# Kernel tuning notes

Measured on AMD Instinct MI355X. Metric: run time of the kernel, lower is better.

The kernel has to match this reference:

```python
import jax, jax.numpy as jnp
import numpy as np

BN_EPS = 1e-5
K = 3  # kernel size


def conv2d(x, w, b, pad):
    y = jax.lax.conv_general_dilated(
        x, w, window_strides=(1, 1), padding=[(pad, pad), (pad, pad)],
        dimension_numbers=('NCHW', 'OIHW', 'NCHW'))
    return y + b[None, :, None, None]


def setup_inputs() -> dict:
    key = jax.random.key(0)
    ks = jax.random.split(key, 4)
    B, C, H, W, O = 8, 256, 64, 64, 256
    x = jax.random.normal(ks[0], (B, C, H, W), dtype=jnp.float32)
    # offset/mask conv: 3*dg*k*k = 27 out channels; small init -> small offsets
    w_off = jax.random.normal(ks[1], (27, C, K, K), dtype=jnp.float32) * 0.01
    b_off = jnp.zeros((27,), dtype=jnp.float32)
    # main deformable conv weight/bias
    w = jax.random.normal(ks[2], (O, C, K, K), dtype=jnp.float32) * 0.05
    b = jnp.zeros((O,), dtype=jnp.float32)
    # BatchNorm (inference) params / running stats
    gamma = jnp.ones((O,), dtype=jnp.float32)
    beta = jnp.zeros((O,), dtype=jnp.float32)
    run_mean = jnp.zeros((O,), dtype=jnp.float32)
    run_var = jnp.ones((O,), dtype=jnp.float32)
    return {"x": x, "w_off": w_off, "b_off": b_off, "w": w, "b": b,
            "gamma": gamma, "beta": beta, "run_mean": run_mean, "run_var": run_var}


def _dcn_bn_relu(x, w_off, b_off, w, b, gamma, beta, run_mean, run_var):
    B, C, H, W = x.shape
    KK = K * K
    # offset + modulation mask (DCNv2): channels [0:9]=dy, [9:18]=dx, [18:27]=mask
    om = conv2d(x, w_off, b_off, pad=1)            # [B, 27, H, W]
    dy, dx = om[:, :KK], om[:, KK:2 * KK]          # [B, 9, H, W]
    mod = jax.nn.sigmoid(om[:, 2 * KK:])           # [B, 9, H, W]

    ky, kx = jnp.meshgrid(jnp.arange(K), jnp.arange(K), indexing='ij')
    # base sampling grid: out pixel + dilation*(k - center), padding=1
    base_y = jnp.arange(H, dtype=jnp.float32)[None, :, None] - 1.0 + ky.reshape(KK, 1, 1)
    base_x = jnp.arange(W, dtype=jnp.float32)[None, None, :] - 1.0 + kx.reshape(KK, 1, 1)
    py = base_y[None] + dy                          # [B, 9, H, W]
    px = base_x[None] + dx

    y0 = jnp.floor(py); x0 = jnp.floor(px)
    fy = py - y0; fx = px - x0
    y0 = y0.astype(jnp.int32); x0 = x0.astype(jnp.int32)

    x_flat = x.reshape(B, C, H * W)
    gather = jax.vmap(lambda xf, idx: xf[:, idx])   # ([C,HW],[9,H,W]) -> [C,9,H,W]

    def corner(yi, xi, wgt):
        valid = (yi >= 0) & (yi < H) & (xi >= 0) & (xi < W)
        idx = jnp.clip(yi, 0, H - 1) * W + jnp.clip(xi, 0, W - 1)
        val = gather(x_flat, idx)                   # [B, C, 9, H, W]
        return val * (wgt * valid.astype(wgt.dtype))[:, None]

    sampled = (corner(y0,     x0,     (1 - fy) * (1 - fx))
               + corner(y0,     x0 + 1, (1 - fy) * fx)
               + corner(y0 + 1, x0,     fy * (1 - fx))
               + corner(y0 + 1, x0 + 1, fy * fx))    # [B, C, 9, H, W]
    sampled = sampled * mod[:, None]                 # modulation

    O = w.shape[0]
    out = jnp.einsum('bckhw,ock->bohw', sampled, w.reshape(O, C, KK))
    out = out + b[None, :, None, None]

    # BatchNorm2d (inference) + ReLU
    inv = gamma / jnp.sqrt(run_var + BN_EPS)
    out = out * inv[None, :, None, None] + (beta - run_mean * inv)[None, :, None, None]
    return jax.nn.relu(out)


def reference(x, w_off, b_off, w, b, gamma, beta, run_mean, run_var):
    return _dcn_bn_relu(x, w_off, b_off, w, b, gamma, beta, run_mean, run_var)
```

## Files before the change

kernel.cpp:

```cpp
#include <hip/hip_runtime.h>
#include <math.h>

#define B_   8
#define C_   256
#define H_   64
#define W_   64
#define O_   256
#define KK_  9
#define CK_  2304
#define HW_  4096
#define BN_EPS 1e-5f

typedef __bf16 bf16x8 __attribute__((ext_vector_type(8)));
typedef float  f32x4  __attribute__((ext_vector_type(4)));

static __device__ __forceinline__ unsigned short f2bf(float f) {
    unsigned int u = __float_as_uint(f);
    unsigned int r = (u + 0x7fffu + ((u >> 16) & 1u)) >> 16;
    return (unsigned short)r;
}
static __device__ __forceinline__ float bflo(unsigned int u) {
    return __uint_as_float(u << 16);
}
static __device__ __forceinline__ float bfhi(unsigned int u) {
    return __uint_as_float(u & 0xffff0000u);
}
static __device__ __forceinline__ unsigned int pack2bf(float a, float b) {
    return (unsigned int)f2bf(a) | ((unsigned int)f2bf(b) << 16);
}

__global__ __launch_bounds__(256) void prep_kernel(
    const float* __restrict__ x, const float* __restrict__ w,
    const float* __restrict__ w_off,
    unsigned short* __restrict__ xT, unsigned short* __restrict__ wKf,
    unsigned short* __restrict__ wof)
{
    int blk = blockIdx.x;
    if (blk < 2048) {
        __shared__ float tile[64][65];
        const int b   = blk & 7;
        const int ct  = (blk >> 3) & 3;
        const int hwt = blk >> 5;
        const int c0  = ct * 64, hw0 = hwt * 64;
        const int tl  = threadIdx.x & 63, tg = threadIdx.x >> 6;
#pragma unroll
        for (int r = 0; r < 16; ++r) {
            int c_l = tg + r * 4;
            tile[c_l][tl] = x[((size_t)(b * C_ + c0 + c_l)) * HW_ + hw0 + tl];
        }
        __syncthreads();
#pragma unroll
        for (int r = 0; r < 16; ++r) {
            int hw_l = tg + r * 4;
            xT[((size_t)(b * HW_ + hw0 + hw_l)) * C_ + c0 + tl] = f2bf(tile[tl][hw_l]);
        }
    } else if (blk < 2048 + 2304) {
        int idx = (blk - 2048) * 256 + threadIdx.x;
        int o   = idx / CK_;
        int rem = idx - o * CK_;
        int c   = rem / 9;
        int tap = rem - c * 9;
        int NT  = o >> 4, n16 = o & 15;
        int kap = tap * 256 + c;
        int KC  = kap >> 5, kr = kap & 31;
        int lane = ((kr >> 3) << 4) | n16, e = kr & 7;
        wKf[((size_t)(NT * 72 + KC) * 64 + lane) * 8 + e] = f2bf(w[idx]);
    } else {
        int idx = (blk - 4352) * 256 + threadIdx.x;
        int NT  = idx / 36864;
        int r   = idx - NT * 36864;
        int KC  = r >> 9;
        int r2  = r & 511;
        int lane = r2 >> 3, e = r2 & 7;
        int n16 = lane & 15, q = lane >> 4;
        int o   = NT * 16 + n16;
        int kap = KC * 32 + q * 8 + e;
        int tap = kap >> 8, c = kap & 255;
        wof[idx] = (o < 27) ? f2bf(w_off[(o * C_ + c) * KK_ + tap])
                            : (unsigned short)0;
    }
}

__global__ __launch_bounds__(512) void offset_mfma_kernel(
    const unsigned short* __restrict__ xT, const unsigned short* __restrict__ wof,
    const float* __restrict__ b_off, float* __restrict__ om)
{
    __shared__ unsigned short rowbuf[66 * 264];

    const int blk = blockIdx.x;
    const int b = blk & 7, h = blk >> 3;
    const int tid = threadIdx.x, lane = tid & 63, wv = tid >> 6;
    const int mi = wv & 3, nj = wv >> 2;
    const int m16 = lane & 15, q = lane >> 4;

    f32x4 acc = {0.f, 0.f, 0.f, 0.f};
    const uint4* wof4 = (const uint4*)wof;

    for (int r = 0; r < 3; ++r) {
        const int hh = h - 1 + r;
        const bool vr = (hh >= 0) && (hh < H_);
        __syncthreads();
        if (vr) {
            const uint4* src = (const uint4*)&xT[((size_t)(b * HW_ + hh * W_)) * C_];
#pragma unroll
            for (int i = 0; i < 8; ++i) {
                int idx8 = i * 512 + tid;
                int px = idx8 >> 5, c8 = (idx8 & 31) * 8;
                *(uint4*)&rowbuf[(px + 1) * 264 + c8] = src[idx8];
            }
        }
        if (tid < 33) {
            *(uint4*)&rowbuf[tid * 8] = make_uint4(0u, 0u, 0u, 0u);
        } else if (tid >= 256 && tid < 289) {
            *(uint4*)&rowbuf[65 * 264 + (tid - 256) * 8] = make_uint4(0u, 0u, 0u, 0u);
        }
        __syncthreads();
        if (vr) {
            for (int s = 0; s < 3; ++s) {
                const unsigned short* arow = &rowbuf[(mi * 16 + m16 + s) * 264 + q * 8];
#pragma unroll
                for (int cc = 0; cc < 8; ++cc) {
                    bf16x8 a = *(const bf16x8*)&arow[cc * 32];
                    const int KC = (r * 3 + s) * 8 + cc;
                    uint4 braw = wof4[(size_t)(nj * 72 + KC) * 64 + lane];
                    acc = __builtin_amdgcn_mfma_f32_16x16x32_bf16(
                        a, __builtin_bit_cast(bf16x8, braw), acc, 0, 0, 0);
                }
            }
        }
    }

    const int t = nj * 16 + m16;
    if (t < 27) {
        const float bo = b_off[t];
        float s0 = acc[0] + bo, s1 = acc[1] + bo, s2 = acc[2] + bo, s3 = acc[3] + bo;
        if (t >= 18) {
            s0 = 1.f / (1.f + expf(-s0));
            s1 = 1.f / (1.f + expf(-s1));
            s2 = 1.f / (1.f + expf(-s2));
            s3 = 1.f / (1.f + expf(-s3));
        }
        float4 rr; rr.x = s0; rr.y = s1; rr.z = s2; rr.w = s3;
        *(float4*)&om[((size_t)(b * 27 + t)) * HW_ + h * W_ + mi * 16 + q * 4] = rr;
    }
}

__global__ __launch_bounds__(512, 4) void dcn_mfma_kernel(
    const unsigned short* __restrict__ xT, const float* __restrict__ om,
    const unsigned short* __restrict__ wKf,
    const float* __restrict__ bias, const float* __restrict__ gamma,
    const float* __restrict__ beta, const float* __restrict__ rmean,
    const float* __restrict__ rvar, float* __restrict__ out)
{
    __shared__ float4 wgtv[576];
    __shared__ int4   idxv[576];
    __shared__ __align__(16) unsigned short Abuf[8][4][64][8];

    const int blk = blockIdx.x;
    const int b = blk & 7, h = blk >> 3;
    const int tid = threadIdx.x, lane = tid & 63, wv = tid >> 6;

    for (int i = tid; i < 576; i += 512) {
        int p = i / 9, t = i - p * 9;
        const int pos = h * W_ + p;
        float dy = om[(b * 27 +      t) * HW_ + pos];
        float dx = om[(b * 27 +  9 + t) * HW_ + pos];
        float md = om[(b * 27 + 18 + t) * HW_ + pos];
        float py = (float)(h - 1 + t / 3) + dy;
        float px = (float)(p - 1 + t % 3) + dx;
        float y0f = floorf(py), x0f = floorf(px);
        int   y0 = (int)y0f,    x0 = (int)x0f;
        float fy = py - y0f,    fx = px - x0f;
        int y0c = min(max(y0,     0), H_ - 1), y1c = min(max(y0 + 1, 0), H_ - 1);
        int x0c = min(max(x0,     0), W_ - 1), x1c = min(max(x0 + 1, 0), W_ - 1);
        float vy0 = (y0     >= 0 && y0     < H_) ? 1.f : 0.f;
        float vy1 = (y0 + 1 >= 0 && y0 + 1 < H_) ? 1.f : 0.f;
        float vx0 = (x0     >= 0 && x0     < W_) ? 1.f : 0.f;
        float vx1 = (x0 + 1 >= 0 && x0 + 1 < W_) ? 1.f : 0.f;
        wgtv[i] = make_float4((1.f - fy) * (1.f - fx) * vy0 * vx0 * md,
                              (1.f - fy) * fx         * vy0 * vx1 * md,
                              fy         * (1.f - fx) * vy1 * vx0 * md,
                              fy         * fx         * vy1 * vx1 * md);
        const int rowb = (b * HW_) * (C_ * 2);
        idxv[i] = make_int4(rowb + (y0c * W_ + x0c) * (C_ * 2),
                            rowb + (y0c * W_ + x1c) * (C_ * 2),
                            rowb + (y1c * W_ + x0c) * (C_ * 2),
                            rowb + (y1c * W_ + x1c) * (C_ * 2));
    }
    __syncthreads();

    f32x4 acc[4][2];
#pragma unroll
    for (int mi = 0; mi < 4; ++mi)
#pragma unroll
        for (int nj = 0; nj < 2; ++nj)
#pragma unroll
            for (int r = 0; r < 4; ++r) acc[mi][nj][r] = 0.f;

    const uint4* wKf4 = (const uint4*)wKf;
    const char*  xTb  = (const char*)xT;

    const int s_cc = lane >> 3;
    const int s_q2 = (lane >> 1) & 3;
    const int s_j0 = (lane & 1) * 4;
    const int s_xr = (s_q2 << 1) ^ s_cc;
    const int s_mi = wv >> 1;
    const int s_pb = (wv & 1) * 8;
    const int loff = lane * 8;

    const int r_row = lane ^ ((lane >> 4) << 1);

    for (int tap = 0; tap < 9; ++tap) {
        uint2 pk[8];
#pragma unroll
        for (int pp = 0; pp < 8; ++pp) {
            const int p = wv * 8 + pp;
            const int4   iq = idxv[p * 9 + tap];
            const float4 wq = wgtv[p * 9 + tap];
            const uint2 k0 = *(const uint2*)(xTb + iq.x + loff);
            const uint2 k1 = *(const uint2*)(xTb + iq.y + loff);
            const uint2 k2 = *(const uint2*)(xTb + iq.z + loff);
            const uint2 k3 = *(const uint2*)(xTb + iq.w + loff);
            float g0 = wq.x*bflo(k0.x) + wq.y*bflo(k1.x) + wq.z*bflo(k2.x) + wq.w*bflo(k3.x);
            float g1 = wq.x*bfhi(k0.x) + wq.y*bfhi(k1.x) + wq.z*bfhi(k2.x) + wq.w*bfhi(k3.x);
            float g2 = wq.x*bflo(k0.y) + wq.y*bflo(k1.y) + wq.z*bflo(k2.y) + wq.w*bflo(k3.y);
            float g3 = wq.x*bfhi(k0.y) + wq.y*bfhi(k1.y) + wq.z*bfhi(k2.y) + wq.w*bfhi(k3.y);
            pk[pp].x = pack2bf(g0, g1);
            pk[pp].y = pack2bf(g2, g3);
        }

        __syncthreads();
#pragma unroll
        for (int pp = 0; pp < 8; ++pp) {
            const int P   = s_pb + pp;
            const int row = (P ^ s_xr) | (s_q2 << 4);
            *(uint2*)&Abuf[s_cc][s_mi][row][s_j0] = pk[pp];
        }
        __syncthreads();

#pragma unroll
        for (int cc = 0; cc < 8; ++cc) {
            const int KC = tap * 8 + cc;
            const int rr = r_row ^ cc;
            uint4 braw[2];
#pragma unroll
            for (int nj = 0; nj < 2; ++nj)
                braw[nj] = wKf4[(size_t)((wv * 2 + nj) * 72 + KC) * 64 + lane];
            bf16x8 a[4];
#pragma unroll
            for (int mi = 0; mi < 4; ++mi)
                a[mi] = *(const bf16x8*)&Abuf[cc][mi][rr][0];
#pragma unroll
            for (int nj = 0; nj < 2; ++nj) {
                bf16x8 bb = __builtin_bit_cast(bf16x8, braw[nj]);
#pragma unroll
                for (int mi = 0; mi < 4; ++mi)
                    acc[mi][nj] = __builtin_amdgcn_mfma_f32_16x16x32_bf16(
                        a[mi], bb, acc[mi][nj], 0, 0, 0);
            }
        }
    }

#pragma unroll
    for (int nj = 0; nj < 2; ++nj) {
        const int o = wv * 32 + nj * 16 + (lane & 15);
        const float inv = gamma[o] * rsqrtf(rvar[o] + BN_EPS);
        const float sh  = beta[o] + (bias[o] - rmean[o]) * inv;
        float* ob = out + ((size_t)(b * O_ + o)) * HW_ + h * W_;
#pragma unroll
        for (int mi = 0; mi < 4; ++mi) {
            f32x4 v = acc[mi][nj];
            float4 r;
            r.x = fmaxf(v[0] * inv + sh, 0.f);
            r.y = fmaxf(v[1] * inv + sh, 0.f);
            r.z = fmaxf(v[2] * inv + sh, 0.f);
            r.w = fmaxf(v[3] * inv + sh, 0.f);
            *(float4*)&ob[mi * 16 + (lane >> 4) * 4] = r;
        }
    }
}

extern "C" void kernel_launch(void* const* d_in, const int* in_sizes, int n_in,
                              void* d_out, int out_size, void* d_ws, size_t ws_size,
                              hipStream_t stream) {
    const float* x     = (const float*)d_in[0];
    const float* w_off = (const float*)d_in[1];
    const float* b_off = (const float*)d_in[2];
    const float* w     = (const float*)d_in[3];
    const float* bias  = (const float*)d_in[4];
    const float* gamma = (const float*)d_in[5];
    const float* beta  = (const float*)d_in[6];
    const float* rmean = (const float*)d_in[7];
    const float* rvar  = (const float*)d_in[8];
    float* out = (float*)d_out;

    float*          om  = (float*)d_ws;
    unsigned short* wKf = (unsigned short*)(om + 884736);
    unsigned short* wof = wKf + 589824;
    unsigned short* xT  = wof + 73728;

    prep_kernel<<<4640, 256, 0, stream>>>(x, w, w_off, xT, wKf, wof);
    offset_mfma_kernel<<<512, 512, 0, stream>>>(xT, wof, b_off, om);
    dcn_mfma_kernel<<<512, 512, 0, stream>>>(
        xT, om, wKf, bias, gamma, beta, rmean, rvar, out);
}
```

Measured before the change: 184.0 us.

## Fuse offset conv into DCN kernel and keep transposed input in fp32

Merges the offset/mask convolution into the main deformable-conv kernel, so offsets live in shared memory instead of a global round trip, and drops one launch. The transposed input is now stored as fp32 rather than bf16. The bilinear gather reads fp32 directly and rounds once to bf16 with a cheaper perm-based packing. This doubles the transposed-input footprint and gather bytes, and it raises shared memory per block, which may cut occupancy.

New measurement: 190.8 us. 1.04x slower.

```diff
diff --git a/kernel.cpp b/kernel.cpp
--- a/kernel.cpp
+++ b/kernel.cpp
@@ -19,20 +19,16 @@
     unsigned int r = (u + 0x7fffu + ((u >> 16) & 1u)) >> 16;
     return (unsigned short)r;
 }
-static __device__ __forceinline__ float bflo(unsigned int u) {
-    return __uint_as_float(u << 16);
-}
-static __device__ __forceinline__ float bfhi(unsigned int u) {
-    return __uint_as_float(u & 0xffff0000u);
-}
-static __device__ __forceinline__ unsigned int pack2bf(float a, float b) {
-    return (unsigned int)f2bf(a) | ((unsigned int)f2bf(b) << 16);
+static __device__ __forceinline__ unsigned int packbf2(float lo, float hi) {
+    unsigned int ul = __float_as_uint(lo) + 0x8000u;
+    unsigned int uh = __float_as_uint(hi) + 0x8000u;
+    return __builtin_amdgcn_perm(uh, ul, 0x07060302u);
 }
 
 __global__ __launch_bounds__(256) void prep_kernel(
     const float* __restrict__ x, const float* __restrict__ w,
     const float* __restrict__ w_off,
-    unsigned short* __restrict__ xT, unsigned short* __restrict__ wKf,
+    float* __restrict__ xF, unsigned short* __restrict__ wKf,
     unsigned short* __restrict__ wof)
 {
     int blk = blockIdx.x;
@@ -52,7 +48,7 @@
 #pragma unroll
         for (int r = 0; r < 16; ++r) {
             int hw_l = tg + r * 4;
-            xT[((size_t)(b * HW_ + hw0 + hw_l)) * C_ + c0 + tl] = f2bf(tile[tl][hw_l]);
+            xF[((size_t)(b * HW_ + hw0 + hw_l)) * C_ + c0 + tl] = tile[tl][hw_l];
         }
     } else if (blk < 2048 + 2304) {
         int idx = (blk - 2048) * 256 + threadIdx.x;
@@ -81,91 +77,95 @@
     }
 }
 
-__global__ __launch_bounds__(512) void offset_mfma_kernel(
-    const unsigned short* __restrict__ xT, const unsigned short* __restrict__ wof,
-    const float* __restrict__ b_off, float* __restrict__ om)
-{
-    __shared__ unsigned short rowbuf[66 * 264];
-
-    const int blk = blockIdx.x;
-    const int b = blk & 7, h = blk >> 3;
-    const int tid = threadIdx.x, lane = tid & 63, wv = tid >> 6;
-    const int mi = wv & 3, nj = wv >> 2;
-    const int m16 = lane & 15, q = lane >> 4;
-
-    f32x4 acc = {0.f, 0.f, 0.f, 0.f};
-    const uint4* wof4 = (const uint4*)wof;
-
-    for (int r = 0; r < 3; ++r) {
-        const int hh = h - 1 + r;
-        const bool vr = (hh >= 0) && (hh < H_);
-        __syncthreads();
-        if (vr) {
-            const uint4* src = (const uint4*)&xT[((size_t)(b * HW_ + hh * W_)) * C_];
-#pragma unroll
-            for (int i = 0; i < 8; ++i) {
-                int idx8 = i * 512 + tid;
-                int px = idx8 >> 5, c8 = (idx8 & 31) * 8;
-                *(uint4*)&rowbuf[(px + 1) * 264 + c8] = src[idx8];
-            }
-        }
-        if (tid < 33) {
-            *(uint4*)&rowbuf[tid * 8] = make_uint4(0u, 0u, 0u, 0u);
-        } else if (tid >= 256 && tid < 289) {
-            *(uint4*)&rowbuf[65 * 264 + (tid - 256) * 8] = make_uint4(0u, 0u, 0u, 0u);
-        }
-        __syncthreads();
-        if (vr) {
-            for (int s = 0; s < 3; ++s) {
-                const unsigned short* arow = &rowbuf[(mi * 16 + m16 + s) * 264 + q * 8];
-#pragma unroll
-                for (int cc = 0; cc < 8; ++cc) {
-                    bf16x8 a = *(const bf16x8*)&arow[cc * 32];
-                    const int KC = (r * 3 + s) * 8 + cc;
-                    uint4 braw = wof4[(size_t)(nj * 72 + KC) * 64 + lane];
-                    acc = __builtin_amdgcn_mfma_f32_16x16x32_bf16(
-                        a, __builtin_bit_cast(bf16x8, braw), acc, 0, 0, 0);
-                }
-            }
-        }
-    }
-
-    const int t = nj * 16 + m16;
-    if (t < 27) {
-        const float bo = b_off[t];
-        float s0 = acc[0] + bo, s1 = acc[1] + bo, s2 = acc[2] + bo, s3 = acc[3] + bo;
-        if (t >= 18) {
-            s0 = 1.f / (1.f + expf(-s0));
-            s1 = 1.f / (1.f + expf(-s1));
-            s2 = 1.f / (1.f + expf(-s2));
-            s3 = 1.f / (1.f + expf(-s3));
-        }
-        float4 rr; rr.x = s0; rr.y = s1; rr.z = s2; rr.w = s3;
-        *(float4*)&om[((size_t)(b * 27 + t)) * HW_ + h * W_ + mi * 16 + q * 4] = rr;
-    }
-}
-
-__global__ __launch_bounds__(512, 4) void dcn_mfma_kernel(
-    const unsigned short* __restrict__ xT, const float* __restrict__ om,
-    const unsigned short* __restrict__ wKf,
+__global__ __launch_bounds__(512, 4) void dcn_fused_kernel(
+    const float* __restrict__ xF, const unsigned short* __restrict__ wKf,
+    const unsigned short* __restrict__ wof, const float* __restrict__ b_off,
     const float* __restrict__ bias, const float* __restrict__ gamma,
     const float* __restrict__ beta, const float* __restrict__ rmean,
     const float* __restrict__ rvar, float* __restrict__ out)
 {
-    __shared__ float4 wgtv[576];
-    __shared__ int4   idxv[576];
-    __shared__ __align__(16) unsigned short Abuf[8][4][64][8];
+    __shared__ __align__(16) unsigned char smem[74528];
+    unsigned short* rowbuf = (unsigned short*)smem;
+    float4*         wgtv   = (float4*)smem;
+    int4*           idxv   = (int4*)(smem + 9216);
+    typedef float OmbT[27][64];
+    OmbT& omb = *(OmbT*)(smem + 34848);
+    typedef unsigned short AbufT[8][4][64][8];
+    AbufT& Abuf = *(AbufT*)(smem + 41760);
 
     const int blk = blockIdx.x;
     const int b = blk & 7, h = blk >> 3;
     const int tid = threadIdx.x, lane = tid & 63, wv = tid >> 6;
+    const int m16 = lane & 15, q = lane >> 4;
+
+    if (tid < 33) {
+        *(uint4*)&rowbuf[tid * 8] = make_uint4(0u, 0u, 0u, 0u);
+    } else if (tid >= 256 && tid < 289) {
+        *(uint4*)&rowbuf[65 * 264 + (tid - 256) * 8] = make_uint4(0u, 0u, 0u, 0u);
+    }
+
+    const int mi_a = wv & 3, nj_a = wv >> 2;
+    f32x4 oacc = {0.f, 0.f, 0.f, 0.f};
+    const uint4* wof4 = (const uint4*)wof;
+
+    for (int r = 0; r < 3; ++r) {
+        const int hh = h - 1 + r;
+        const bool vr = (hh >= 0) && (hh < H_);
+        __syncthreads();
+        if (vr) {
+            const float* src = xF + ((size_t)(b * HW_ + hh * W_)) * C_;
+#pragma unroll
+            for (int i = 0; i < 4; ++i) {
+                const int idx8 = i * 512 + tid;
+                f32x4 v0 = *(const f32x4*)(src + idx8 * 8);
+                f32x4 v1 = *(const f32x4*)(src + idx8 * 8 + 4);
+                uint4 pk;
+                pk.x = packbf2(v0[0], v0[1]);
+                pk.y = packbf2(v0[2], v0[3]);
+                pk.z = packbf2(v1[0], v1[1]);
+                pk.w = packbf2(v1[2], v1[3]);
+                const int px = idx8 >> 5, c8 = (idx8 & 31) * 8;
+                *(uint4*)&rowbuf[(px + 1) * 264 + c8] = pk;
+            }
+        }
+        __syncthreads();
+        if (vr) {
+#pragma unroll
+            for (int s = 0; s < 3; ++s) {
+                const unsigned short* arow = &rowbuf[(mi_a * 16 + m16 + s) * 264 + q * 8];
+#pragma unroll
+                for (int cc = 0; cc < 8; ++cc) {
+                    bf16x8 a = *(const bf16x8*)&arow[cc * 32];
+                    uint4 braw = wof4[(size_t)(nj_a * 72 + (r * 3 + s) * 8 + cc) * 64 + lane];
+                    oacc = __builtin_amdgcn_mfma_f32_16x16x32_bf16(
+                        a, __builtin_bit_cast(bf16x8, braw), oacc, 0, 0, 0);
+                }
+            }
+        }
+    }
+    {
+        const int t = nj_a * 16 + m16;
+        if (t < 27) {
+            const float bo = b_off[t];
+            float s0 = oacc[0] + bo, s1 = oacc[1] + bo,
+                  s2 = oacc[2] + bo, s3 = oacc[3] + bo;
+            if (t >= 18) {
+                s0 = 1.f / (1.f + expf(-s0));
+                s1 = 1.f / (1.f + expf(-s1));
+                s2 = 1.f / (1.f + expf(-s2));
+                s3 = 1.f / (1.f + expf(-s3));
+            }
+            float4 rr; rr.x = s0; rr.y = s1; rr.z = s2; rr.w = s3;
+            *(float4*)&omb[t][mi_a * 16 + q * 4] = rr;
+        }
+    }
+    __syncthreads();
 
     for (int i = tid; i < 576; i += 512) {
         int p = i / 9, t = i - p * 9;
-        const int pos = h * W_ + p;
-        float dy = om[(b * 27 +      t) * HW_ + pos];
-        float dx = om[(b * 27 +  9 + t) * HW_ + pos];
-        float md = om[(b * 27 + 18 + t) * HW_ + pos];
+        float dy = omb[t][p];
+        float dx = omb[t + 9][p];
+        float md = omb[t + 18][p];
         float py = (float)(h - 1 + t / 3) + dy;
         float px = (float)(p - 1 + t % 3) + dx;
         float y0f = floorf(py), x0f = floorf(px);
@@ -181,11 +181,11 @@
                               (1.f - fy) * fx         * vy0 * vx1 * md,
                               fy         * (1.f - fx) * vy1 * vx0 * md,
                               fy         * fx         * vy1 * vx1 * md);
-        const int rowb = (b * HW_) * (C_ * 2);
-        idxv[i] = make_int4(rowb + (y0c * W_ + x0c) * (C_ * 2),
-                            rowb + (y0c * W_ + x1c) * (C_ * 2),
-                            rowb + (y1c * W_ + x0c) * (C_ * 2),
-                            rowb + (y1c * W_ + x1c) * (C_ * 2));
+        const int rowb = (b * HW_) * (C_ * 4);
+        idxv[i] = make_int4(rowb + (y0c * W_ + x0c) * (C_ * 4),
+                            rowb + (y0c * W_ + x1c) * (C_ * 4),
+                            rowb + (y1c * W_ + x0c) * (C_ * 4),
+                            rowb + (y1c * W_ + x1c) * (C_ * 4));
     }
     __syncthreads();
 
@@ -198,7 +198,7 @@
             for (int r = 0; r < 4; ++r) acc[mi][nj][r] = 0.f;
 
     const uint4* wKf4 = (const uint4*)wKf;
-    const char*  xTb  = (const char*)xT;
+    const char*  xFb  = (const char*)xF;
 
     const int s_cc = lane >> 3;
     const int s_q2 = (lane >> 1) & 3;
@@ -206,7 +206,7 @@
     const int s_xr = (s_q2 << 1) ^ s_cc;
     const int s_mi = wv >> 1;
     const int s_pb = (wv & 1) * 8;
-    const int loff = lane * 8;
+    const int loff = lane * 16;
 
     const int r_row = lane ^ ((lane >> 4) << 1);
 
@@ -217,16 +217,13 @@
             const int p = wv * 8 + pp;
             const int4   iq = idxv[p * 9 + tap];
             const float4 wq = wgtv[p * 9 + tap];
-            const uint2 k0 = *(const uint2*)(xTb + iq.x + loff);
-            const uint2 k1 = *(const uint2*)(xTb + iq.y + loff);
-            const uint2 k2 = *(const uint2*)(xTb + iq.z + loff);
-            const uint2 k3 = *(const uint2*)(xTb + iq.w + loff);
-            float g0 = wq.x*bflo(k0.x) + wq.y*bflo(k1.x) + wq.z*bflo(k2.x) + wq.w*bflo(k3.x);
-            float g1 = wq.x*bfhi(k0.x) + wq.y*bfhi(k1.x) + wq.z*bfhi(k2.x) + wq.w*bfhi(k3.x);
-            float g2 = wq.x*bflo(k0.y) + wq.y*bflo(k1.y) + wq.z*bflo(k2.y) + wq.w*bflo(k3.y);
-            float g3 = wq.x*bfhi(k0.y) + wq.y*bfhi(k1.y) + wq.z*bfhi(k2.y) + wq.w*bfhi(k3.y);
-            pk[pp].x = pack2bf(g0, g1);
-            pk[pp].y = pack2bf(g2, g3);
+            f32x4 c0 = *(const f32x4*)(xFb + iq.x + loff);
+            f32x4 c1 = *(const f32x4*)(xFb + iq.y + loff);
+            f32x4 c2 = *(const f32x4*)(xFb + iq.z + loff);
+            f32x4 c3 = *(const f32x4*)(xFb + iq.w + loff);
+            f32x4 g = c0 * wq.x + c1 * wq.y + c2 * wq.z + c3 * wq.w;
+            pk[pp].x = packbf2(g[0], g[1]);
+            pk[pp].y = packbf2(g[2], g[3]);
         }
 
         __syncthreads();
@@ -294,13 +291,11 @@
     const float* rvar  = (const float*)d_in[8];
     float* out = (float*)d_out;
 
-    float*          om  = (float*)d_ws;
-    unsigned short* wKf = (unsigned short*)(om + 884736);
+    float*          xF  = (float*)d_ws;
+    unsigned short* wKf = (unsigned short*)(xF + 8388608);
     unsigned short* wof = wKf + 589824;
-    unsigned short* xT  = wof + 73728;
-
-    prep_kernel<<<4640, 256, 0, stream>>>(x, w, w_off, xT, wKf, wof);
-    offset_mfma_kernel<<<512, 512, 0, stream>>>(xT, wof, b_off, om);
-    dcn_mfma_kernel<<<512, 512, 0, stream>>>(
-        xT, om, wKf, bias, gamma, beta, rmean, rvar, out);
-}
+
+    prep_kernel<<<4640, 256, 0, stream>>>(x, w, w_off, xF, wKf, wof);
+    dcn_fused_kernel<<<512, 512, 0, stream>>>(
+        xF, wKf, wof, b_off, bias, gamma, beta, rmean, rvar, out);
+}
```
